# Kernel tuning notes

Measured on AMD Instinct MI355X. Metric: run time of the kernel, lower is better.

Reference implementation:

```python
import jax, jax.numpy as jnp
import numpy as np

DIM, HID, SEQ = 768, 2048, 4096
LR, MOM, WD, THRESH = 1e-3, 0.9, 0.01, 0.1


def _net(p, x):
    W1, b1, W2, b2, W3, b3, W4, b4 = p
    h = jax.nn.relu(x @ W1 + b1)
    h = jax.nn.relu(h @ W2 + b2)
    h = jax.nn.relu(h @ W3 + b3)
    return h @ W4 + b4


def _loss(p, t):
    # t: [dim]; token.unsqueeze(0) then mse_loss (mean over all elements)
    pred = _net(p, t[None, :])
    return jnp.mean((pred - t[None, :]) ** 2)


def _ttt(params, x):
    toks = x[::4]  # `if i % 4 != 0: continue`

    def step(carry, t):
        p, buf, inited = carry
        g = jax.grad(_loss)(p, t)
        surprise = sum(jnp.linalg.norm(gi) for gi in jax.tree_util.tree_leaves(g))
        # momentum buffer: first observation initializes it
        buf_new = jnp.where(inited, MOM * buf + (1.0 - MOM) * surprise, surprise)

        def upd(q):
            qd = jax.tree_util.tree_map(lambda w: w * (1.0 - WD), q)  # weight decay
            g2 = jax.grad(_loss)(qd, t)                                # fresh fwd/bwd
            return jax.tree_util.tree_map(lambda w, gi: w - LR * gi, qd, g2)  # SGD step

        p_new = jax.lax.cond(buf_new > THRESH, upd, lambda q: q, p)
        return (p_new, buf_new, jnp.bool_(True)), None

    (pf, _, _), _ = jax.lax.scan(step, (params, jnp.float32(0.0), jnp.bool_(False)), toks)
    return pf


def setup_inputs() -> dict:
    key = jax.random.key(0)
    ks = jax.random.split(key, 5)

    def lin(k, fi, fo):
        kw, kb = jax.random.split(k)
        w = jax.random.normal(kw, (fi, fo), jnp.float32) / np.sqrt(fi).astype(np.float32)
        b = jax.random.normal(kb, (fo,), jnp.float32) * 0.01
        return w, b

    W1, b1 = lin(ks[0], DIM, HID)
    W2, b2 = lin(ks[1], HID, HID)
    W3, b3 = lin(ks[2], HID, HID)
    W4, b4 = lin(ks[3], HID, DIM)
    x = jax.random.normal(ks[4], (SEQ, DIM), jnp.float32)
    return dict(x=x, W1=W1, b1=b1, W2=W2, b2=b2, W3=W3, b3=b3, W4=W4, b4=b4, do_ttt=1)


def reference(x, W1, b1, W2, b2, W3, b3, W4, b4, do_ttt):
    params = (W1, b1, W2, b2, W3, b3, W4, b4)
    if do_ttt:
        params = _ttt(params, x)
    out = _net(params, x)            # eval pass over full sequence
    return out.mean(axis=0, keepdims=True)  # memory_summary [1, dim]
```

## Files before the change

kernel.cpp:

```cpp
#include <hip/hip_runtime.h>
#include <cstddef>

#define LRC 0.001f
#define DEC 0.99f

typedef float f32x4 __attribute__((ext_vector_type(4)));

static const size_t OFF_H1F = 376832;
static const size_t OFF_H2F = 380928;
static const size_t OFF_H2Q = 382976;
static const size_t OFF_H3F = 385024;
static const size_t OFF_H3Q = 387072;
static const size_t OFF_D4F = 389120;
static const size_t OFF_D4Q = 389888;
static const size_t OFF_D3F = 390656;
static const size_t OFF_D3Q = 392704;
static const size_t OFF_D2F = 394752;
static const size_t OFF_D2Q = 396800;
static const size_t OFF_SL4 = 398848;
static const size_t OFF_D1Q = 400896;
static const size_t OFF_NSQ = 402944;
static const size_t OFF_SL3 = 402960;
static const size_t OFF_SL2 = 403216;
static const size_t OFF_SL1 = 403472;
static const size_t OFF_MSUM = 403732;
static const size_t OFF_HA  = 428308;
static const size_t OFF_HB  = 2525460;

#define ST0  0
#define ST1  2048
#define ST2  4096
#define ST3  6144
#define SD4F 8192
#define SD4Q 8960
#define SRED 9728
#define SCND 10240
#define SBUF 10244
#define SCOND 10245
#define SB4  10248
#define SSQ  10256
#define SWRP 10264
#define SWRQ 10288

__device__ __forceinline__ float clf(const float* p) {
    return __hip_atomic_load(p, __ATOMIC_RELAXED, __HIP_MEMORY_SCOPE_AGENT);
}
__device__ __forceinline__ void csf(float* p, float v) {
    __hip_atomic_store(p, v, __ATOMIC_RELAXED, __HIP_MEMORY_SCOPE_AGENT);
}
__device__ __forceinline__ f32x4 cl4(const float* p) {
    f32x4 r;
    asm volatile("global_load_dwordx4 %0, %1, off sc0 sc1" : "=&v"(r) : "v"(p) : "memory");
    return r;
}
__device__ __forceinline__ void cs4(float* p, f32x4 v) {
    asm volatile("global_store_dwordx4 %0, %1, off sc0 sc1" :: "v"(p), "v"(v) : "memory");
}
__device__ __forceinline__ void vwait() {
    asm volatile("s_waitcnt vmcnt(0)" ::: "memory");
    __builtin_amdgcn_sched_barrier(0);
}

__device__ __forceinline__ float dot4(const f32x4 a, const f32x4 b) {
    float s = a.x * b.x; s += a.y * b.y; s += a.z * b.z; s += a.w * b.w; return s;
}
__device__ __forceinline__ int swz(int p) { return p ^ (((p >> 5) & 7) << 2); }

__device__ __forceinline__ void updc(f32x4& wv, const f32x4 a, float dq) {
    wv.x = DEC * wv.x - (LRC * a.x) * dq;
    wv.y = DEC * wv.y - (LRC * a.y) * dq;
    wv.z = DEC * wv.z - (LRC * a.z) * dq;
    wv.w = DEC * wv.w - (LRC * a.w) * dq;
}
__device__ __forceinline__ void updr(f32x4& wv, float u, const f32x4 dv) {
    wv.x = DEC * wv.x - u * dv.x;
    wv.y = DEC * wv.y - u * dv.y;
    wv.z = DEC * wv.z - u * dv.z;
    wv.w = DEC * wv.w - u * dv.w;
}

__device__ __forceinline__ float block_reduce_512s(float v, float* red) {
    int t = threadIdx.x;
    red[t] = v;
    __syncthreads();
    for (int st = 256; st > 0; st >>= 1) {
        if (t < st) red[t] += red[t + st];
        __syncthreads();
    }
    float r = red[0];
    __syncthreads();
    return r;
}

__device__ __forceinline__ void gbar(unsigned* bar) {
    asm volatile("s_waitcnt vmcnt(0) lgkmcnt(0)" ::: "memory");
    __syncthreads();
    if (threadIdx.x == 0) {
        unsigned g = __hip_atomic_load(bar, __ATOMIC_RELAXED, __HIP_MEMORY_SCOPE_AGENT);
        unsigned* grp = bar + 64 + ((blockIdx.x >> 4) << 5);
        bool released = false;
        if (__hip_atomic_fetch_add(grp, 1u, __ATOMIC_RELAXED, __HIP_MEMORY_SCOPE_AGENT) == 15u) {
            if (__hip_atomic_fetch_add(bar + 32, 1u, __ATOMIC_RELAXED, __HIP_MEMORY_SCOPE_AGENT) == 15u) {
#pragma unroll
                for (int i = 0; i < 16; ++i)
                    __hip_atomic_store(bar + 64 + (i << 5), 0u, __ATOMIC_RELAXED, __HIP_MEMORY_SCOPE_AGENT);
                __hip_atomic_store(bar + 32, 0u, __ATOMIC_RELAXED, __HIP_MEMORY_SCOPE_AGENT);
                __hip_atomic_store(bar, g + 1u, __ATOMIC_RELEASE, __HIP_MEMORY_SCOPE_AGENT);
                released = true;
            }
        }
        if (!released) {
            while (__hip_atomic_load(bar, __ATOMIC_RELAXED, __HIP_MEMORY_SCOPE_AGENT) == g)
                __builtin_amdgcn_s_sleep(2);
            (void)__hip_atomic_load(bar, __ATOMIC_ACQUIRE, __HIP_MEMORY_SCOPE_AGENT);
        }
    }
    __syncthreads();
}

__global__ __launch_bounds__(1024) void k_zero(unsigned* __restrict__ bar) {
    bar[threadIdx.x] = 0u;
}

#define L3M(M) M(0) M(1) M(2)
#define L8M(M) M(0) M(1) M(2) M(3) M(4) M(5) M(6) M(7)
#define LDS_SW(buf, i) (*(const f32x4*)(smem + (buf) + swz(32 * lane + 4 * (i))))
#define LDS_D4(buf, i) (*(const f32x4*)(smem + (buf) + 12 * lane + 4 * (i)))

__global__ void __attribute__((amdgpu_flat_work_group_size(512, 512), amdgpu_waves_per_eu(2, 2)))
k_scan(const float* __restrict__ x,
       float* __restrict__ W1g, float* __restrict__ b1g,
       float* __restrict__ W2g, float* __restrict__ b2g,
       float* __restrict__ W3g, float* __restrict__ b3g,
       float* __restrict__ W4g, float* __restrict__ b4g,
       float* __restrict__ wsf,
       const int* __restrict__ flag) {
    if (*flag == 0) return;
    __shared__ __align__(16) float smem[16896];
    unsigned* bar = (unsigned*)(wsf + OFF_HA);
    const int b = blockIdx.x, tid = threadIdx.x;
    const int w = tid >> 6, lane = tid & 63;
    const int jw = 8 * b + w;
    const int c3 = 3 * b;
    const int t4 = tid * 4;

    f32x4 w1c0, w1c1, w1c2;
    f32x4 w2c0, w2c1, w2c2, w2c3, w2c4, w2c5, w2c6, w2c7;
    f32x4 w3c0, w3c1, w3c2, w3c3, w3c4, w3c5, w3c6, w3c7;
    f32x4 w4c0, w4c1, w4c2;
    f32x4 w4r0, w4r1, w4r2;
    f32x4 w2r0, w2r1, w2r2, w2r3, w2r4, w2r5, w2r6, w2r7;
    f32x4 w3r0, w3r1, w3r2, w3r3, w3r4, w3r5, w3r6, w3r7;

#define LD_COL(dst, Wg, ld, row0, col) { f32x4 t; \
    t.x = Wg[(size_t)((row0) + 0) * (ld) + (col)]; \
    t.y = Wg[(size_t)((row0) + 1) * (ld) + (col)]; \
    t.z = Wg[(size_t)((row0) + 2) * (ld) + (col)]; \
    t.w = Wg[(size_t)((row0) + 3) * (ld) + (col)]; dst = t; }
#define LDW1C(i) LD_COL(w1c##i, W1g, 2048, 12 * lane + 4 * (i), jw)
    L3M(LDW1C)
#undef LDW1C
#define LDW2C(i) LD_COL(w2c##i, W2g, 2048, 32 * lane + 4 * (i), jw)
    L8M(LDW2C)
#undef LDW2C
#define LDW3C(i) LD_COL(w3c##i, W3g, 2048, 32 * lane + 4 * (i), jw)
    L8M(LDW3C)
#undef LDW3C
#define LDW4C(i) LD_COL(w4c##i, W4g, 768, 4 * tid, c3 + (i))
    L3M(LDW4C)
#undef LDW4C
#define LDW4R(i) w4r##i = *(const f32x4*)(W4g + (size_t)jw * 768 + 12 * lane + 4 * (i));
    L3M(LDW4R)
#undef LDW4R
#define LDW2R(i) w2r##i = *(const f32x4*)(W2g + (size_t)jw * 2048 + 32 * lane + 4 * (i));
    L8M(LDW2R)
#undef LDW2R
#define LDW3R(i) w3r##i = *(const f32x4*)(W3g + (size_t)jw * 2048 + 32 * lane + 4 * (i));
    L8M(LDW3R)
#undef LDW3R
    if (tid == 0) smem[SBUF] = 0.f;

    for (int s = 0; s < 1024; ++s) {
        const float* xt = x + (size_t)s * 3072;
        const float* xprev = x + (size_t)(s > 0 ? s - 1 : 0) * 3072;

        float cond = 0.f;
        if (s > 0) {
            if (w < 4) {
                const float* sl = wsf + (w == 0 ? OFF_SL1 : w == 1 ? OFF_SL2 : w == 2 ? OFF_SL3 : OFF_SL4);
                float v = clf(sl + lane) + clf(sl + lane + 64) + clf(sl + lane + 128) + clf(sl + lane + 192);
#pragma unroll
                for (int off = 32; off > 0; off >>= 1) v += __shfl_down(v, off);
                if (lane == 0) smem[SCND + w] = v;
            }
            __syncthreads();
            if (tid == 0) {
                float nd1 = sqrtf(smem[SCND + 0]), nd2 = sqrtf(smem[SCND + 1]);
                float nd3 = sqrtf(smem[SCND + 2]), nd4 = sqrtf(smem[SCND + 3]);
                float nx = sqrtf(clf(wsf + OFF_NSQ + 0));
                float nh1 = sqrtf(clf(wsf + OFF_NSQ + 1));
                float nh2 = sqrtf(clf(wsf + OFF_NSQ + 2));
                float nh3 = sqrtf(clf(wsf + OFF_NSQ + 3));
                float surprise = nx * nd1 + nd1 + nh1 * nd2 + nd2 + nh2 * nd3 + nd3 + nh3 * nd4 + nd4;
                float bufold = smem[SBUF];
                float bufnew = (s == 1) ? surprise : (0.9f * bufold + 0.1f * surprise);
                smem[SBUF] = bufnew;
                smem[SCOND] = (bufnew > 0.1f) ? 1.f : 0.f;
            }
            __syncthreads();
            cond = smem[SCOND];
        }
        float b1j;
        if (cond != 0.f) {
            f32x4 a0 = cl4(wsf + OFF_H1F + t4);
            f32x4 a1 = cl4(wsf + OFF_H2Q + t4);
            f32x4 a2 = cl4(wsf + OFF_D2Q + t4);
            f32x4 a3 = cl4(wsf + OFF_D3Q + t4);
            f32x4 hq3 = cl4(wsf + OFF_H3Q + t4);
            f32x4 d4s = {0.f, 0.f, 0.f, 0.f};
            if (tid < 192) d4s = cl4(wsf + OFF_D4Q + t4);
            float d1qj = clf(wsf + OFF_D1Q + jw);
            float h3qr = clf(wsf + OFF_H3Q + jw);
            float h2qr = clf(wsf + OFF_H2Q + jw);
            float ob1 = b1g[jw];
            f32x4 xp0 = *(const f32x4*)(xprev + 12 * lane);
            f32x4 xp1 = *(const f32x4*)(xprev + 12 * lane + 4);
            f32x4 xp2 = *(const f32x4*)(xprev + 12 * lane + 8);
            vwait();
            {
                int st = swz(t4);
                *(f32x4*)(smem + ST0 + st) = a0;
                *(f32x4*)(smem + ST1 + st) = a1;
                *(f32x4*)(smem + ST2 + st) = a2;
                *(f32x4*)(smem + ST3 + st) = a3;
            }
            if (tid < 192) *(f32x4*)(smem + SD4Q + t4) = d4s;
            __syncthreads();
            updc(w1c0, xp0, d1qj); updc(w1c1, xp1, d1qj); updc(w1c2, xp2, d1qj);
            {
                float d2qj = smem[ST2 + swz(jw)];
#define UPW2C(i) { f32x4 hf = LDS_SW(ST0, i); f32x4 af; \
                   af.x = DEC * hf.x; af.y = DEC * hf.y; af.z = DEC * hf.z; af.w = DEC * hf.w; \
                   updc(w2c##i, af, d2qj); }
                L8M(UPW2C)
#undef UPW2C
            }
            {
                float d3qj = smem[ST3 + swz(jw)];
#define UPW3C(i) { f32x4 hq = LDS_SW(ST1, i); updc(w3c##i, hq, d3qj); }
                L8M(UPW3C)
#undef UPW3C
            }
            {
                float vq0 = smem[SD4Q + c3 + 0];
                float vq1 = smem[SD4Q + c3 + 1];
                float vq2 = smem[SD4Q + c3 + 2];
                updc(w4c0, hq3, vq0); updc(w4c1, hq3, vq1); updc(w4c2, hq3, vq2);
            }
            {
                float u = LRC * h3qr;
#define UPW4R(i) { f32x4 dv = LDS_D4(SD4Q, i); updr(w4r##i, u, dv); }
                L3M(UPW4R)
#undef UPW4R
            }
            {
                float u = LRC * h2qr;
#define UPW3R(i) { f32x4 dv = LDS_SW(ST3, i); updr(w3r##i, u, dv); }
                L8M(UPW3R)
#undef UPW3R
            }
            {
                float u = LRC * (DEC * smem[ST0 + swz(jw)]);
#define UPW2R(i) { f32x4 dv = LDS_SW(ST2, i); updr(w2r##i, u, dv); }
                L8M(UPW2R)
#undef UPW2R
            }
            b1j = DEC * ob1 - LRC * d1qj;
            if (lane == 0) b1g[jw] = b1j;
        } else {
            b1j = b1g[jw];
        }
        {
            f32x4 x0 = *(const f32x4*)(xt + 12 * lane);
            f32x4 x1 = *(const f32x4*)(xt + 12 * lane + 4);
            f32x4 x2 = *(const f32x4*)(xt + 12 * lane + 8);
            float acc = dot4(w1c0, x0);
            acc += dot4(w1c1, x1);
            acc += dot4(w1c2, x2);
#pragma unroll
            for (int off = 32; off > 0; off >>= 1) acc += __shfl_down(acc, off);
            if (lane == 0) csf(wsf + OFF_H1F + jw, fmaxf(acc + b1j, 0.f));
        }
        gbar(bar);

        {
            f32x4 hv = cl4(wsf + OFF_H1F + t4);
            float ob2 = b2g[jw];
            float d2qjo = (cond != 0.f) ? clf(wsf + OFF_D2Q + jw) : 0.f;
            vwait();
            *(f32x4*)(smem + ST0 + swz(t4)) = hv;
            float b2j = (cond != 0.f) ? (DEC * ob2 - LRC * d2qjo) : ob2;
            if (cond != 0.f && lane == 0) b2g[jw] = b2j;
            __syncthreads();
            float accP = 0.f, accQ = 0.f;
#define PHB(i) { const f32x4 hf = LDS_SW(ST0, i); f32x4 hq; \
                 hq.x = DEC * hf.x; hq.y = DEC * hf.y; hq.z = DEC * hf.z; hq.w = DEC * hf.w; \
                 accP += dot4(w2c##i, hf); accQ += dot4(w2c##i, hq); }
            L8M(PHB)
#undef PHB
#pragma unroll
            for (int off = 32; off > 0; off >>= 1) {
                accP += __shfl_down(accP, off);
                accQ += __shfl_down(accQ, off);
            }
            if (lane == 0) {
                csf(wsf + OFF_H2F + jw, fmaxf(accP + b2j, 0.f));
                csf(wsf + OFF_H2Q + jw, fmaxf(DEC * (accQ + b2j), 0.f));
            }
        }
        gbar(bar);

        {
            f32x4 hfv = cl4(wsf + OFF_H2F + t4);
            f32x4 hqv = cl4(wsf + OFF_H2Q + t4);
            float ob3 = b3g[jw];
            float d3qjo = (cond != 0.f) ? clf(wsf + OFF_D3Q + jw) : 0.f;
            vwait();
            {
                int st = swz(t4);
                *(f32x4*)(smem + ST0 + st) = hfv;
                *(f32x4*)(smem + ST1 + st) = hqv;
            }
            float b3j = (cond != 0.f) ? (DEC * ob3 - LRC * d3qjo) : ob3;
            if (cond != 0.f && lane == 0) b3g[jw] = b3j;
            __syncthreads();
            float accP = 0.f, accQ = 0.f;
#define PHC(i) { const f32x4 hf = LDS_SW(ST0, i); const f32x4 hq = LDS_SW(ST1, i); \
                 accP += dot4(w3c##i, hf); accQ += dot4(w3c##i, hq); }
            L8M(PHC)
#undef PHC
#pragma unroll
            for (int off = 32; off > 0; off >>= 1) {
                accP += __shfl_down(accP, off);
                accQ += __shfl_down(accQ, off);
            }
            if (lane == 0) {
                csf(wsf + OFF_H3F + jw, fmaxf(accP + b3j, 0.f));
                csf(wsf + OFF_H3Q + jw, fmaxf(DEC * (accQ + b3j), 0.f));
            }
        }
        gbar(bar);

        {
            f32x4 hfv = cl4(wsf + OFF_H3F + t4);
            f32x4 hqv = cl4(wsf + OFF_H3Q + t4);
            float tv = 0.f;
            if (tid < 3) {
                float ob4 = b4g[c3 + tid];
                float d4qjo = (cond != 0.f) ? clf(wsf + OFF_D4Q + c3 + tid) : 0.f;
                tv = xt[c3 + tid];
                float bn = (cond != 0.f) ? (DEC * ob4 - LRC * d4qjo) : ob4;
                if (cond != 0.f) b4g[c3 + tid] = bn;
                smem[SB4 + tid] = bn;
            }
            vwait();
            {
                int st = swz(t4);
                *(f32x4*)(smem + ST0 + st) = hfv;
                *(f32x4*)(smem + ST1 + st) = hqv;
            }
            float aP0 = dot4(w4c0, hfv), aP1 = dot4(w4c1, hfv), aP2 = dot4(w4c2, hfv);
            float aQ0 = dot4(w4c0, hqv), aQ1 = dot4(w4c1, hqv), aQ2 = dot4(w4c2, hqv);
#pragma unroll
            for (int off = 32; off > 0; off >>= 1) {
                aP0 += __shfl_down(aP0, off); aP1 += __shfl_down(aP1, off); aP2 += __shfl_down(aP2, off);
                aQ0 += __shfl_down(aQ0, off); aQ1 += __shfl_down(aQ1, off); aQ2 += __shfl_down(aQ2, off);
            }
            if (lane == 0) {
                smem[SWRP + w * 3 + 0] = aP0; smem[SWRP + w * 3 + 1] = aP1; smem[SWRP + w * 3 + 2] = aP2;
                smem[SWRQ + w * 3 + 0] = aQ0; smem[SWRQ + w * 3 + 1] = aQ1; smem[SWRQ + w * 3 + 2] = aQ2;
            }
            __syncthreads();
            if (tid < 3) {
                float zp = 0.f, zq = 0.f;
#pragma unroll
                for (int q = 0; q < 8; ++q) { zp += smem[SWRP + q * 3 + tid]; zq += smem[SWRQ + q * 3 + tid]; }
                float bn = smem[SB4 + tid];
                float d4f = 2.f * ((zp + bn) - tv) * (1.f / 768.f);
                float d4q = 2.f * (DEC * (zq + bn) - tv) * (1.f / 768.f);
                csf(wsf + OFF_D4F + c3 + tid, d4f);
                csf(wsf + OFF_D4Q + c3 + tid, d4q);
                smem[SSQ + tid] = d4f * d4f;
            }
            __syncthreads();
            if (tid == 0) csf(wsf + OFF_SL4 + b, smem[SSQ + 0] + smem[SSQ + 1] + smem[SSQ + 2]);
            if (b >= 1 && b <= 4) {
                float v = 0.f;
                if (b == 4) {
                    if (tid < 192) {
                        f32x4 xv = *(const f32x4*)(xt + t4);
                        v = xv.x * xv.x + xv.y * xv.y + xv.z * xv.z + xv.w * xv.w;
                    }
                } else {
                    const float* src = (b == 1) ? wsf + OFF_H1F : (b == 2) ? wsf + OFF_H2F : wsf + OFF_H3F;
                    f32x4 hh = cl4(src + t4);
                    vwait();
                    v = hh.x * hh.x + hh.y * hh.y + hh.z * hh.z + hh.w * hh.w;
                }
                float sres = block_reduce_512s(v, smem + SRED);
                if (tid == 0) csf(wsf + OFF_NSQ + ((b == 4) ? 0 : b), sres);
            }
        }
        gbar(bar);

        {
            f32x4 p4 = {0.f, 0.f, 0.f, 0.f}, q4 = {0.f, 0.f, 0.f, 0.f};
            if (tid < 192) {
                p4 = cl4(wsf + OFF_D4F + t4);
                q4 = cl4(wsf + OFF_D4Q + t4);
            }
            vwait();
            if (tid < 192) {
                *(f32x4*)(smem + SD4F + t4) = p4;
                *(f32x4*)(smem + SD4Q + t4) = q4;
            }
            __syncthreads();
            float accP = 0.f, accQ = 0.f;
#define PHE(i) { const f32x4 dP = LDS_D4(SD4F, i); const f32x4 dQ = LDS_D4(SD4Q, i); \
                 accP += dot4(w4r##i, dP); accQ += dot4(w4r##i, dQ); }
            L3M(PHE)
#undef PHE
#pragma unroll
            for (int off = 32; off > 0; off >>= 1) {
                accP += __shfl_down(accP, off);
                accQ += __shfl_down(accQ, off);
            }
            if (lane == 0) {
                float dp = (smem[ST0 + swz(jw)] > 0.f) ? accP : 0.f;
                float dq = (smem[ST1 + swz(jw)] > 0.f) ? DEC * accQ : 0.f;
                csf(wsf + OFF_D3F + jw, dp);
                csf(wsf + OFF_D3Q + jw, dq);
                smem[SSQ + w] = dp * dp;
            }
            __syncthreads();
            if (tid == 0) {
                float ss = 0.f;
#pragma unroll
                for (int q = 0; q < 8; ++q) ss += smem[SSQ + q];
                csf(wsf + OFF_SL3 + b, ss);
            }
        }
        gbar(bar);

        {
            f32x4 fP = cl4(wsf + OFF_D3F + t4);
            f32x4 fQ = cl4(wsf + OFF_D3Q + t4);
            float h2fr = clf(wsf + OFF_H2F + jw);
            float h2qr = clf(wsf + OFF_H2Q + jw);
            vwait();
            {
                int st = swz(t4);
                *(f32x4*)(smem + ST2 + st) = fP;
                *(f32x4*)(smem + ST3 + st) = fQ;
            }
            __syncthreads();
            float accP = 0.f, accQ = 0.f;
#define PHF(i) { const f32x4 dP = LDS_SW(ST2, i); const f32x4 dQ = LDS_SW(ST3, i); \
                 accP += dot4(w3r##i, dP); accQ += dot4(w3r##i, dQ); }
            L8M(PHF)
#undef PHF
#pragma unroll
            for (int off = 32; off > 0; off >>= 1) {
                accP += __shfl_down(accP, off);
                accQ += __shfl_down(accQ, off);
            }
            if (lane == 0) {
                float dp = (h2fr > 0.f) ? accP : 0.f;
                float dq = (h2qr > 0.f) ? DEC * accQ : 0.f;
                csf(wsf + OFF_D2F + jw, dp);
                csf(wsf + OFF_D2Q + jw, dq);
                smem[SSQ + w] = dp * dp;
            }
            __syncthreads();
            if (tid == 0) {
                float ss = 0.f;
#pragma unroll
                for (int q = 0; q < 8; ++q) ss += smem[SSQ + q];
                csf(wsf + OFF_SL2 + b, ss);
            }
        }
        gbar(bar);

        {
            f32x4 fP = cl4(wsf + OFF_D2F + t4);
            f32x4 fQ = cl4(wsf + OFF_D2Q + t4);
            float h1fr = clf(wsf + OFF_H1F + jw);
            vwait();
            {
                int st = swz(t4);
                *(f32x4*)(smem + ST0 + st) = fP;
                *(f32x4*)(smem + ST1 + st) = fQ;
            }
            __syncthreads();
            float accP = 0.f, accQ = 0.f;
#define PHG(i) { const f32x4 dP = LDS_SW(ST0, i); const f32x4 dQ = LDS_SW(ST1, i); \
                 accP += dot4(w2r##i, dP); accQ += dot4(w2r##i, dQ); }
            L8M(PHG)
#undef PHG
#pragma unroll
            for (int off = 32; off > 0; off >>= 1) {
                accP += __shfl_down(accP, off);
                accQ += __shfl_down(accQ, off);
            }
            if (lane == 0) {
                float dp = (h1fr > 0.f) ? accP : 0.f;
                float h1qr = DEC * h1fr;
                float dq = (h1qr > 0.f) ? DEC * accQ : 0.f;
                csf(wsf + OFF_D1Q + jw, dq);
                smem[SSQ + w] = dp * dp;
            }
            __syncthreads();
            if (tid == 0) {
                float ss = 0.f;
#pragma unroll
                for (int q = 0; q < 8; ++q) ss += smem[SSQ + q];
                csf(wsf + OFF_SL1 + b, ss);
            }
        }
        gbar(bar);
    }

    {
        if (w < 4) {
            const float* sl = wsf + (w == 0 ? OFF_SL1 : w == 1 ? OFF_SL2 : w == 2 ? OFF_SL3 : OFF_SL4);
            float v = clf(sl + lane) + clf(sl + lane + 64) + clf(sl + lane + 128) + clf(sl + lane + 192);
#pragma unroll
            for (int off = 32; off > 0; off >>= 1) v += __shfl_down(v, off);
            if (lane == 0) smem[SCND + w] = v;
        }
        __syncthreads();
        if (tid == 0) {
            float nd1 = sqrtf(smem[SCND + 0]), nd2 = sqrtf(smem[SCND + 1]);
            float nd3 = sqrtf(smem[SCND + 2]), nd4 = sqrtf(smem[SCND + 3]);
            float nx = sqrtf(clf(wsf + OFF_NSQ + 0));
            float nh1 = sqrtf(clf(wsf + OFF_NSQ + 1));
            float nh2 = sqrtf(clf(wsf + OFF_NSQ + 2));
            float nh3 = sqrtf(clf(wsf + OFF_NSQ + 3));
            float surprise = nx * nd1 + nd1 + nh1 * nd2 + nd2 + nh2 * nd3 + nd3 + nh3 * nd4 + nd4;
            float bufnew = 0.9f * smem[SBUF] + 0.1f * surprise;
            smem[SCOND] = (bufnew > 0.1f) ? 1.f : 0.f;
        }
        __syncthreads();
        if (smem[SCOND] != 0.f) {
            const float* xpE = x + (size_t)1023 * 3072;
            f32x4 a0 = cl4(wsf + OFF_H1F + t4);
            f32x4 a1 = cl4(wsf + OFF_H2Q + t4);
            f32x4 hq3 = cl4(wsf + OFF_H3Q + t4);
            f32x4 d4s = {0.f, 0.f, 0.f, 0.f};
            if (tid < 192) d4s = cl4(wsf + OFF_D4Q + t4);
            float d1qj = clf(wsf + OFF_D1Q + jw);
            float d2qj = clf(wsf + OFF_D2Q + jw);
            float d3qj = clf(wsf + OFF_D3Q + jw);
            f32x4 xp0 = *(const f32x4*)(xpE + 12 * lane);
            f32x4 xp1 = *(const f32x4*)(xpE + 12 * lane + 4);
            f32x4 xp2 = *(const f32x4*)(xpE + 12 * lane + 8);
            vwait();
            {
                int st = swz(t4);
                *(f32x4*)(smem + ST0 + st) = a0;
                *(f32x4*)(smem + ST1 + st) = a1;
            }
            if (tid < 192) *(f32x4*)(smem + SD4Q + t4) = d4s;
            __syncthreads();
            updc(w1c0, xp0, d1qj); updc(w1c1, xp1, d1qj); updc(w1c2, xp2, d1qj);
#define EPW2C(i) { f32x4 hf = LDS_SW(ST0, i); f32x4 af; \
                   af.x = DEC * hf.x; af.y = DEC * hf.y; af.z = DEC * hf.z; af.w = DEC * hf.w; \
                   updc(w2c##i, af, d2qj); }
            L8M(EPW2C)
#undef EPW2C
#define EPW3C(i) { f32x4 hq = LDS_SW(ST1, i); updc(w3c##i, hq, d3qj); }
            L8M(EPW3C)
#undef EPW3C
            {
                float vq0 = smem[SD4Q + c3 + 0];
                float vq1 = smem[SD4Q + c3 + 1];
                float vq2 = smem[SD4Q + c3 + 2];
                updc(w4c0, hq3, vq0); updc(w4c1, hq3, vq1); updc(w4c2, hq3, vq2);
            }
            if (lane == 0) {
                b1g[jw] = DEC * b1g[jw] - LRC * d1qj;
                b2g[jw] = DEC * b2g[jw] - LRC * d2qj;
                b3g[jw] = DEC * b3g[jw] - LRC * d3qj;
            }
            if (tid < 3) b4g[c3 + tid] = DEC * b4g[c3 + tid] - LRC * smem[SD4Q + c3 + tid];
        }
    }

    __syncthreads();
    {
#define WBW2(i) { smem[(32 * lane + 4 * (i) + 0) * 8 + w] = w2c##i.x; \
                  smem[(32 * lane + 4 * (i) + 1) * 8 + w] = w2c##i.y; \
                  smem[(32 * lane + 4 * (i) + 2) * 8 + w] = w2c##i.z; \
                  smem[(32 * lane + 4 * (i) + 3) * 8 + w] = w2c##i.w; }
        L8M(WBW2)
#undef WBW2
        __syncthreads();
#pragma unroll
        for (int r2 = 0; r2 < 4; ++r2) {
            int r = t4 + r2;
            *(f32x4*)(W2g + (size_t)r * 2048 + 8 * b) = *(const f32x4*)(smem + r * 8);
            *(f32x4*)(W2g + (size_t)r * 2048 + 8 * b + 4) = *(const f32x4*)(smem + r * 8 + 4);
        }
        __syncthreads();
    }
    {
#define WBW3(i) { smem[(32 * lane + 4 * (i) + 0) * 8 + w] = w3c##i.x; \
                  smem[(32 * lane + 4 * (i) + 1) * 8 + w] = w3c##i.y; \
                  smem[(32 * lane + 4 * (i) + 2) * 8 + w] = w3c##i.z; \
                  smem[(32 * lane + 4 * (i) + 3) * 8 + w] = w3c##i.w; }
        L8M(WBW3)
#undef WBW3
        __syncthreads();
#pragma unroll
        for (int r2 = 0; r2 < 4; ++r2) {
            int r = t4 + r2;
            *(f32x4*)(W3g + (size_t)r * 2048 + 8 * b) = *(const f32x4*)(smem + r * 8);
            *(f32x4*)(W3g + (size_t)r * 2048 + 8 * b + 4) = *(const f32x4*)(smem + r * 8 + 4);
        }
        __syncthreads();
    }
    {
#define WBW1(i) { smem[(12 * lane + 4 * (i) + 0) * 8 + w] = w1c##i.x; \
                  smem[(12 * lane + 4 * (i) + 1) * 8 + w] = w1c##i.y; \
                  smem[(12 * lane + 4 * (i) + 2) * 8 + w] = w1c##i.z; \
                  smem[(12 * lane + 4 * (i) + 3) * 8 + w] = w1c##i.w; }
        L3M(WBW1)
#undef WBW1
        __syncthreads();
        for (int r = tid; r < 768; r += 512) {
            *(f32x4*)(W1g + (size_t)r * 2048 + 8 * b) = *(const f32x4*)(smem + r * 8);
            *(f32x4*)(W1g + (size_t)r * 2048 + 8 * b + 4) = *(const f32x4*)(smem + r * 8 + 4);
        }
        __syncthreads();
    }
    {
#define WBW4(c) { smem[(4 * tid + 0) * 3 + (c)] = w4c##c.x; \
                  smem[(4 * tid + 1) * 3 + (c)] = w4c##c.y; \
                  smem[(4 * tid + 2) * 3 + (c)] = w4c##c.z; \
                  smem[(4 * tid + 3) * 3 + (c)] = w4c##c.w; }
        L3M(WBW4)
#undef WBW4
        __syncthreads();
#pragma unroll
        for (int r2 = 0; r2 < 4; ++r2) {
            int r = t4 + r2;
            W4g[(size_t)r * 768 + c3 + 0] = smem[r * 3 + 0];
            W4g[(size_t)r * 768 + c3 + 1] = smem[r * 3 + 1];
            W4g[(size_t)r * 768 + c3 + 2] = smem[r * 3 + 2];
        }
    }
}

__global__ __launch_bounds__(256) void k_gemm(const float* __restrict__ A,
                                              const float* __restrict__ W,
                                              const float* __restrict__ bias,
                                              float* __restrict__ C,
                                              int M, int N, int K, int do_relu) {
    __shared__ float sA[16][64];
    __shared__ float sB[16][128];
    int bn = blockIdx.x, bm = blockIdx.y;
    int m0 = bm * 64, n0 = bn * 128;
    int tid = threadIdx.x;
    int tx = tid & 31, ty = tid >> 5;
    float acc[8][4];
#pragma unroll
    for (int i = 0; i < 8; ++i)
#pragma unroll
        for (int j = 0; j < 4; ++j) acc[i][j] = 0.f;

    for (int kt = 0; kt < K; kt += 16) {
        {
            int r = tid >> 2, cc = (tid & 3) * 4;
            const float4 a4 = *(const float4*)(A + (size_t)(m0 + r) * K + kt + cc);
            sA[cc + 0][r] = a4.x; sA[cc + 1][r] = a4.y; sA[cc + 2][r] = a4.z; sA[cc + 3][r] = a4.w;
        }
        {
            int r = tid >> 5, cc = (tid & 31) * 4;
            *(float4*)(&sB[r][cc]) = *(const float4*)(W + (size_t)(kt + r) * N + n0 + cc);
            *(float4*)(&sB[r + 8][cc]) = *(const float4*)(W + (size_t)(kt + r + 8) * N + n0 + cc);
        }
        __syncthreads();
#pragma unroll
        for (int k = 0; k < 16; ++k) {
            float av[8];
#pragma unroll
            for (int i = 0; i < 8; ++i) av[i] = sA[k][ty * 8 + i];
            float bx = sB[k][tx * 4 + 0], by = sB[k][tx * 4 + 1];
            float bz = sB[k][tx * 4 + 2], bw = sB[k][tx * 4 + 3];
#pragma unroll
            for (int i = 0; i < 8; ++i) {
                acc[i][0] += av[i] * bx; acc[i][1] += av[i] * by;
                acc[i][2] += av[i] * bz; acc[i][3] += av[i] * bw;
            }
        }
        __syncthreads();
    }
    float bx = bias[n0 + tx * 4 + 0], by = bias[n0 + tx * 4 + 1];
    float bz = bias[n0 + tx * 4 + 2], bw = bias[n0 + tx * 4 + 3];
#pragma unroll
    for (int i = 0; i < 8; ++i) {
        int m = m0 + ty * 8 + i;
        float4 v;
        v.x = acc[i][0] + bx; v.y = acc[i][1] + by;
        v.z = acc[i][2] + bz; v.w = acc[i][3] + bw;
        if (do_relu) {
            v.x = fmaxf(v.x, 0.f); v.y = fmaxf(v.y, 0.f);
            v.z = fmaxf(v.z, 0.f); v.w = fmaxf(v.w, 0.f);
        }
        *(float4*)(C + (size_t)m * N + n0 + tx * 4) = v;
    }
}

__global__ __launch_bounds__(128) void k_colsum(const float* __restrict__ Y,
                                                float* __restrict__ out) {
    int c = blockIdx.x * 128 + threadIdx.x;
    int r0 = blockIdx.y * 128;
    float s = 0.f;
    for (int r = 0; r < 128; ++r) s += Y[(size_t)(r0 + r) * 768 + c];
    out[blockIdx.y * 768 + c] = s;
}

__global__ __launch_bounds__(768) void k_out(const float* __restrict__ msum,
                                             float* __restrict__ out) {
    int c = threadIdx.x;
    float s = 0.f;
#pragma unroll
    for (int i = 0; i < 32; ++i) s += msum[i * 768 + c];
    out[c] = s * (1.f / 4096.f);
}

extern "C" void kernel_launch(void* const* d_in, const int* in_sizes, int n_in,
                              void* d_out, int out_size, void* d_ws, size_t ws_size,
                              hipStream_t stream) {
    const float* x = (const float*)d_in[0];
    float* W1 = (float*)d_in[1];
    float* b1 = (float*)d_in[2];
    float* W2 = (float*)d_in[3];
    float* b2 = (float*)d_in[4];
    float* W3 = (float*)d_in[5];
    float* b3 = (float*)d_in[6];
    float* W4 = (float*)d_in[7];
    float* b4 = (float*)d_in[8];
    const int* flag = (const int*)d_in[9];
    float* wsf = (float*)d_ws;

    unsigned* bar = (unsigned*)(wsf + OFF_HA);
    k_zero<<<1, 1024, 0, stream>>>(bar);

    k_scan<<<256, 512, 0, stream>>>(x, W1, b1, W2, b2, W3, b3, W4, b4, wsf, flag);

    float* HA = wsf + OFF_HA;
    float* HB = wsf + OFF_HB;
    for (int ch = 0; ch < 4; ++ch) {
        const float* Xc = x + (size_t)ch * 1024 * 768;
        k_gemm<<<dim3(16, 16), 256, 0, stream>>>(Xc, W1, b1, HA, 1024, 2048, 768, 1);
        k_gemm<<<dim3(16, 16), 256, 0, stream>>>(HA, W2, b2, HB, 1024, 2048, 2048, 1);
        k_gemm<<<dim3(16, 16), 256, 0, stream>>>(HB, W3, b3, HA, 1024, 2048, 2048, 1);
        k_gemm<<<dim3(6, 16), 256, 0, stream>>>(HA, W4, b4, HB, 1024, 768, 2048, 0);
        k_colsum<<<dim3(6, 8), 128, 0, stream>>>(HB, wsf + OFF_MSUM + (size_t)ch * 8 * 768);
    }
    k_out<<<1, 768, 0, stream>>>(wsf + OFF_MSUM, (float*)d_out);
}
```

Measured before the change: 66.14 ms.

## Keep per-step activations and deltas resident in LDS instead of reloading from global

The shared-memory layout is reorganized so that activation vectors (h1, h2, h3) and backprop deltas (d2, d3, d4, d1 per-wave) stay in dedicated LDS slots across phases of the persistent scan kernel. The weight-update phase and several bias and norm computations now read these from LDS rather than issuing coherent global loads plus a vwait and a staging barrier. This is meant to cut global round-trips and one block-wide sync per step on the serial critical path. It raises LDS usage per block and adds an extra vmcnt wait inside the grid barrier.

```diff
diff --git a/kernel.cpp b/kernel.cpp
--- a/kernel.cpp
+++ b/kernel.cpp
@@ -27,20 +27,25 @@
 static const size_t OFF_HA  = 428308;
 static const size_t OFF_HB  = 2525460;
 
-#define ST0  0
-#define ST1  2048
-#define ST2  4096
-#define ST3  6144
-#define SD4F 8192
-#define SD4Q 8960
-#define SRED 9728
-#define SCND 10240
-#define SBUF 10244
-#define SCOND 10245
-#define SB4  10248
-#define SSQ  10256
-#define SWRP 10264
-#define SWRQ 10288
+#define PH1F 0
+#define PH2F 2048
+#define PH2Q 4096
+#define PH3Q 6144
+#define PD2Q 8192
+#define PD3Q 10240
+#define PD4Q 12288
+#define SD4F 13056
+#define ST0  13824
+#define ST2  15872
+#define SRED 17920
+#define SCND 18432
+#define SBUF 18436
+#define SCOND 18437
+#define SB4  18440
+#define SSQ  18448
+#define SWRP 18456
+#define SWRQ 18480
+#define PD1W 18504
 
 __device__ __forceinline__ float clf(const float* p) {
     return __hip_atomic_load(p, __ATOMIC_RELAXED, __HIP_MEMORY_SCOPE_AGENT);
@@ -52,9 +57,6 @@
     f32x4 r;
     asm volatile("global_load_dwordx4 %0, %1, off sc0 sc1" : "=&v"(r) : "v"(p) : "memory");
     return r;
-}
-__device__ __forceinline__ void cs4(float* p, f32x4 v) {
-    asm volatile("global_store_dwordx4 %0, %1, off sc0 sc1" :: "v"(p), "v"(v) : "memory");
 }
 __device__ __forceinline__ void vwait() {
     asm volatile("s_waitcnt vmcnt(0)" ::: "memory");
@@ -97,6 +99,7 @@
     __syncthreads();
     if (threadIdx.x == 0) {
         unsigned g = __hip_atomic_load(bar, __ATOMIC_RELAXED, __HIP_MEMORY_SCOPE_AGENT);
+        asm volatile("s_waitcnt vmcnt(0)" ::: "memory");
         unsigned* grp = bar + 64 + ((blockIdx.x >> 4) << 5);
         bool released = false;
         if (__hip_atomic_fetch_add(grp, 1u, __ATOMIC_RELAXED, __HIP_MEMORY_SCOPE_AGENT) == 15u) {
@@ -127,16 +130,16 @@
 #define LDS_SW(buf, i) (*(const f32x4*)(smem + (buf) + swz(32 * lane + 4 * (i))))
 #define LDS_D4(buf, i) (*(const f32x4*)(smem + (buf) + 12 * lane + 4 * (i)))
 
-__global__ void __attribute__((amdgpu_flat_work_group_size(512, 512), amdgpu_waves_per_eu(2, 2)))
-k_scan(const float* __restrict__ x,
-       float* __restrict__ W1g, float* __restrict__ b1g,
-       float* __restrict__ W2g, float* __restrict__ b2g,
-       float* __restrict__ W3g, float* __restrict__ b3g,
-       float* __restrict__ W4g, float* __restrict__ b4g,
-       float* __restrict__ wsf,
-       const int* __restrict__ flag) {
+__global__ __attribute__((amdgpu_flat_work_group_size(512, 512), amdgpu_waves_per_eu(2, 2)))
+void k_scan(const float* __restrict__ x,
+            float* __restrict__ W1g, float* __restrict__ b1g,
+            float* __restrict__ W2g, float* __restrict__ b2g,
+            float* __restrict__ W3g, float* __restrict__ b3g,
+            float* __restrict__ W4g, float* __restrict__ b4g,
+            float* __restrict__ wsf,
+            const int* __restrict__ flag) {
     if (*flag == 0) return;
-    __shared__ __align__(16) float smem[16896];
+    __shared__ __align__(16) float smem[18512];
     unsigned* bar = (unsigned*)(wsf + OFF_HA);
     const int b = blockIdx.x, tid = threadIdx.x;
     const int w = tid >> 6, lane = tid & 63;
@@ -212,66 +215,48 @@
         }
         float b1j;
         if (cond != 0.f) {
-            f32x4 a0 = cl4(wsf + OFF_H1F + t4);
-            f32x4 a1 = cl4(wsf + OFF_H2Q + t4);
-            f32x4 a2 = cl4(wsf + OFF_D2Q + t4);
-            f32x4 a3 = cl4(wsf + OFF_D3Q + t4);
-            f32x4 hq3 = cl4(wsf + OFF_H3Q + t4);
-            f32x4 d4s = {0.f, 0.f, 0.f, 0.f};
-            if (tid < 192) d4s = cl4(wsf + OFF_D4Q + t4);
-            float d1qj = clf(wsf + OFF_D1Q + jw);
-            float h3qr = clf(wsf + OFF_H3Q + jw);
-            float h2qr = clf(wsf + OFF_H2Q + jw);
             float ob1 = b1g[jw];
             f32x4 xp0 = *(const f32x4*)(xprev + 12 * lane);
             f32x4 xp1 = *(const f32x4*)(xprev + 12 * lane + 4);
             f32x4 xp2 = *(const f32x4*)(xprev + 12 * lane + 8);
-            vwait();
-            {
-                int st = swz(t4);
-                *(f32x4*)(smem + ST0 + st) = a0;
-                *(f32x4*)(smem + ST1 + st) = a1;
-                *(f32x4*)(smem + ST2 + st) = a2;
-                *(f32x4*)(smem + ST3 + st) = a3;
-            }
-            if (tid < 192) *(f32x4*)(smem + SD4Q + t4) = d4s;
-            __syncthreads();
+            float d1qj = smem[PD1W + w];
             updc(w1c0, xp0, d1qj); updc(w1c1, xp1, d1qj); updc(w1c2, xp2, d1qj);
             {
-                float d2qj = smem[ST2 + swz(jw)];
-#define UPW2C(i) { f32x4 hf = LDS_SW(ST0, i); f32x4 af; \
+                float d2qj = smem[PD2Q + swz(jw)];
+#define UPW2C(i) { f32x4 hf = LDS_SW(PH1F, i); f32x4 af; \
                    af.x = DEC * hf.x; af.y = DEC * hf.y; af.z = DEC * hf.z; af.w = DEC * hf.w; \
                    updc(w2c##i, af, d2qj); }
                 L8M(UPW2C)
 #undef UPW2C
             }
             {
-                float d3qj = smem[ST3 + swz(jw)];
-#define UPW3C(i) { f32x4 hq = LDS_SW(ST1, i); updc(w3c##i, hq, d3qj); }
+                float d3qj = smem[PD3Q + swz(jw)];
+#define UPW3C(i) { f32x4 hq = LDS_SW(PH2Q, i); updc(w3c##i, hq, d3qj); }
                 L8M(UPW3C)
 #undef UPW3C
             }
             {
-                float vq0 = smem[SD4Q + c3 + 0];
-                float vq1 = smem[SD4Q + c3 + 1];
-                float vq2 = smem[SD4Q + c3 + 2];
+                f32x4 hq3 = *(const f32x4*)(smem + PH3Q + swz(t4));
+                float vq0 = smem[PD4Q + c3 + 0];
+                float vq1 = smem[PD4Q + c3 + 1];
+                float vq2 = smem[PD4Q + c3 + 2];
                 updc(w4c0, hq3, vq0); updc(w4c1, hq3, vq1); updc(w4c2, hq3, vq2);
             }
             {
-                float u = LRC * h3qr;
-#define UPW4R(i) { f32x4 dv = LDS_D4(SD4Q, i); updr(w4r##i, u, dv); }
+                float u = LRC * smem[PH3Q + swz(jw)];
+#define UPW4R(i) { f32x4 dv = LDS_D4(PD4Q, i); updr(w4r##i, u, dv); }
                 L3M(UPW4R)
 #undef UPW4R
             }
             {
-                float u = LRC * h2qr;
-#define UPW3R(i) { f32x4 dv = LDS_SW(ST3, i); updr(w3r##i, u, dv); }
+                float u = LRC * smem[PH2Q + swz(jw)];
+#define UPW3R(i) { f32x4 dv = LDS_SW(PD3Q, i); updr(w3r##i, u, dv); }
                 L8M(UPW3R)
 #undef UPW3R
             }
             {
-                float u = LRC * (DEC * smem[ST0 + swz(jw)]);
-#define UPW2R(i) { f32x4 dv = LDS_SW(ST2, i); updr(w2r##i, u, dv); }
+                float u = LRC * (DEC * smem[PH1F + swz(jw)]);
+#define UPW2R(i) { f32x4 dv = LDS_SW(PD2Q, i); updr(w2r##i, u, dv); }
                 L8M(UPW2R)
 #undef UPW2R
             }
@@ -296,14 +281,14 @@
         {
             f32x4 hv = cl4(wsf + OFF_H1F + t4);
             float ob2 = b2g[jw];
-            float d2qjo = (cond != 0.f) ? clf(wsf + OFF_D2Q + jw) : 0.f;
+            float d2qjo = (cond != 0.f) ? smem[PD2Q + swz(jw)] : 0.f;
             vwait();
-            *(f32x4*)(smem + ST0 + swz(t4)) = hv;
+            *(f32x4*)(smem + PH1F + swz(t4)) = hv;
             float b2j = (cond != 0.f) ? (DEC * ob2 - LRC * d2qjo) : ob2;
             if (cond != 0.f && lane == 0) b2g[jw] = b2j;
             __syncthreads();
             float accP = 0.f, accQ = 0.f;
-#define PHB(i) { const f32x4 hf = LDS_SW(ST0, i); f32x4 hq; \
+#define PHB(i) { const f32x4 hf = LDS_SW(PH1F, i); f32x4 hq; \
                  hq.x = DEC * hf.x; hq.y = DEC * hf.y; hq.z = DEC * hf.z; hq.w = DEC * hf.w; \
                  accP += dot4(w2c##i, hf); accQ += dot4(w2c##i, hq); }
             L8M(PHB)
@@ -324,18 +309,18 @@
             f32x4 hfv = cl4(wsf + OFF_H2F + t4);
             f32x4 hqv = cl4(wsf + OFF_H2Q + t4);
             float ob3 = b3g[jw];
-            float d3qjo = (cond != 0.f) ? clf(wsf + OFF_D3Q + jw) : 0.f;
+            float d3qjo = (cond != 0.f) ? smem[PD3Q + swz(jw)] : 0.f;
             vwait();
             {
                 int st = swz(t4);
-                *(f32x4*)(smem + ST0 + st) = hfv;
-                *(f32x4*)(smem + ST1 + st) = hqv;
+                *(f32x4*)(smem + PH2F + st) = hfv;
+                *(f32x4*)(smem + PH2Q + st) = hqv;
             }
             float b3j = (cond != 0.f) ? (DEC * ob3 - LRC * d3qjo) : ob3;
             if (cond != 0.f && lane == 0) b3g[jw] = b3j;
             __syncthreads();
             float accP = 0.f, accQ = 0.f;
-#define PHC(i) { const f32x4 hf = LDS_SW(ST0, i); const f32x4 hq = LDS_SW(ST1, i); \
+#define PHC(i) { const f32x4 hf = LDS_SW(PH2F, i); const f32x4 hq = LDS_SW(PH2Q, i); \
                  accP += dot4(w3c##i, hf); accQ += dot4(w3c##i, hq); }
             L8M(PHC)
 #undef PHC
@@ -357,7 +342,7 @@
             float tv = 0.f;
             if (tid < 3) {
                 float ob4 = b4g[c3 + tid];
-                float d4qjo = (cond != 0.f) ? clf(wsf + OFF_D4Q + c3 + tid) : 0.f;
+                float d4qjo = (cond != 0.f) ? smem[PD4Q + c3 + tid] : 0.f;
                 tv = xt[c3 + tid];
                 float bn = (cond != 0.f) ? (DEC * ob4 - LRC * d4qjo) : ob4;
                 if (cond != 0.f) b4g[c3 + tid] = bn;
@@ -367,7 +352,7 @@
             {
                 int st = swz(t4);
                 *(f32x4*)(smem + ST0 + st) = hfv;
-                *(f32x4*)(smem + ST1 + st) = hqv;
+                *(f32x4*)(smem + PH3Q + st) = hqv;
             }
             float aP0 = dot4(w4c0, hfv), aP1 = dot4(w4c1, hfv), aP2 = dot4(w4c2, hfv);
             float aQ0 = dot4(w4c0, hqv), aQ1 = dot4(w4c1, hqv), aQ2 = dot4(w4c2, hqv);
@@ -402,9 +387,8 @@
                         v = xv.x * xv.x + xv.y * xv.y + xv.z * xv.z + xv.w * xv.w;
                     }
                 } else {
-                    const float* src = (b == 1) ? wsf + OFF_H1F : (b == 2) ? wsf + OFF_H2F : wsf + OFF_H3F;
-                    f32x4 hh = cl4(src + t4);
-                    vwait();
+                    const int so = (b == 1) ? PH1F : (b == 2) ? PH2F : ST0;
+                    f32x4 hh = *(const f32x4*)(smem + so + swz(t4));
                     v = hh.x * hh.x + hh.y * hh.y + hh.z * hh.z + hh.w * hh.w;
                 }
                 float sres = block_reduce_512s(v, smem + SRED);
@@ -422,11 +406,11 @@
             vwait();
             if (tid < 192) {
                 *(f32x4*)(smem + SD4F + t4) = p4;
-                *(f32x4*)(smem + SD4Q + t4) = q4;
+                *(f32x4*)(smem + PD4Q + t4) = q4;
             }
             __syncthreads();
             float accP = 0.f, accQ = 0.f;
-#define PHE(i) { const f32x4 dP = LDS_D4(SD4F, i); const f32x4 dQ = LDS_D4(SD4Q, i); \
+#define PHE(i) { const f32x4 dP = LDS_D4(SD4F, i); const f32x4 dQ = LDS_D4(PD4Q, i); \
                  accP += dot4(w4r##i, dP); accQ += dot4(w4r##i, dQ); }
             L3M(PHE)
 #undef PHE
@@ -437,7 +421,7 @@
             }
             if (lane == 0) {
                 float dp = (smem[ST0 + swz(jw)] > 0.f) ? accP : 0.f;
-                float dq = (smem[ST1 + swz(jw)] > 0.f) ? DEC * accQ : 0.f;
+                float dq = (smem[PH3Q + swz(jw)] > 0.f) ? DEC * accQ : 0.f;
                 csf(wsf + OFF_D3F + jw, dp);
                 csf(wsf + OFF_D3Q + jw, dq);
                 smem[SSQ + w] = dp * dp;
@@ -455,17 +439,17 @@
         {
             f32x4 fP = cl4(wsf + OFF_D3F + t4);
             f32x4 fQ = cl4(wsf + OFF_D3Q + t4);
-            float h2fr = clf(wsf + OFF_H2F + jw);
-            float h2qr = clf(wsf + OFF_H2Q + jw);
+            float h2fr = smem[PH2F + swz(jw)];
+            float h2qr = smem[PH2Q + swz(jw)];
             vwait();
             {
                 int st = swz(t4);
                 *(f32x4*)(smem + ST2 + st) = fP;
-                *(f32x4*)(smem + ST3 + st) = fQ;
+                *(f32x4*)(smem + PD3Q + st) = fQ;
             }
             __syncthreads();
             float accP = 0.f, accQ = 0.f;
-#define PHF(i) { const f32x4 dP = LDS_SW(ST2, i); const f32x4 dQ = LDS_SW(ST3, i); \
+#define PHF(i) { const f32x4 dP = LDS_SW(ST2, i); const f32x4 dQ = LDS_SW(PD3Q, i); \
                  accP += dot4(w3r##i, dP); accQ += dot4(w3r##i, dQ); }
             L8M(PHF)
 #undef PHF
@@ -494,16 +478,16 @@
         {
             f32x4 fP = cl4(wsf + OFF_D2F + t4);
             f32x4 fQ = cl4(wsf + OFF_D2Q + t4);
-            float h1fr = clf(wsf + OFF_H1F + jw);
+            float h1fr = smem[PH1F + swz(jw)];
             vwait();
             {
                 int st = swz(t4);
                 *(f32x4*)(smem + ST0 + st) = fP;
-                *(f32x4*)(smem + ST1 + st) = fQ;
+                *(f32x4*)(smem + PD2Q + st) = fQ;
             }
             __syncthreads();
             float accP = 0.f, accQ = 0.f;
-#define PHG(i) { const f32x4 dP = LDS_SW(ST0, i); const f32x4 dQ = LDS_SW(ST1, i); \
+#define PHG(i) { const f32x4 dP = LDS_SW(ST0, i); const f32x4 dQ = LDS_SW(PD2Q, i); \
                  accP += dot4(w2r##i, dP); accQ += dot4(w2r##i, dQ); }
             L8M(PHG)
 #undef PHG
@@ -517,6 +501,7 @@
                 float h1qr = DEC * h1fr;
                 float dq = (h1qr > 0.f) ? DEC * accQ : 0.f;
                 csf(wsf + OFF_D1Q + jw, dq);
+                smem[PD1W + w] = dq;
                 smem[SSQ + w] = dp * dp;
             }
             __syncthreads();
@@ -553,38 +538,26 @@
         __syncthreads();
         if (smem[SCOND] != 0.f) {
             const float* xpE = x + (size_t)1023 * 3072;
-            f32x4 a0 = cl4(wsf + OFF_H1F + t4);
-            f32x4 a1 = cl4(wsf + OFF_H2Q + t4);
-            f32x4 hq3 = cl4(wsf + OFF_H3Q + t4);
-            f32x4 d4s = {0.f, 0.f, 0.f, 0.f};
-            if (tid < 192) d4s = cl4(wsf + OFF_D4Q + t4);
-            float d1qj = clf(wsf + OFF_D1Q + jw);
-            float d2qj = clf(wsf + OFF_D2Q + jw);
-            float d3qj = clf(wsf + OFF_D3Q + jw);
             f32x4 xp0 = *(const f32x4*)(xpE + 12 * lane);
             f32x4 xp1 = *(const f32x4*)(xpE + 12 * lane + 4);
             f32x4 xp2 = *(const f32x4*)(xpE + 12 * lane + 8);
-            vwait();
-            {
-                int st = swz(t4);
-                *(f32x4*)(smem + ST0 + st) = a0;
-                *(f32x4*)(smem + ST1 + st) = a1;
-            }
-            if (tid < 192) *(f32x4*)(smem + SD4Q + t4) = d4s;
-            __syncthreads();
+            float d1qj = smem[PD1W + w];
             updc(w1c0, xp0, d1qj); updc(w1c1, xp1, d1qj); updc(w1c2, xp2, d1qj);
-#define EPW2C(i) { f32x4 hf = LDS_SW(ST0, i); f32x4 af; \
+            float d2qj = smem[PD2Q + swz(jw)];
+            float d3qj = smem[PD3Q + swz(jw)];
+#define EPW2C(i) { f32x4 hf = LDS_SW(PH1F, i); f32x4 af; \
                    af.x = DEC * hf.x; af.y = DEC * hf.y; af.z = DEC * hf.z; af.w = DEC * hf.w; \
                    updc(w2c##i, af, d2qj); }
             L8M(EPW2C)
 #undef EPW2C
-#define EPW3C(i) { f32x4 hq = LDS_SW(ST1, i); updc(w3c##i, hq, d3qj); }
+#define EPW3C(i) { f32x4 hq = LDS_SW(PH2Q, i); updc(w3c##i, hq, d3qj); }
             L8M(EPW3C)
 #undef EPW3C
             {
-                float vq0 = smem[SD4Q + c3 + 0];
-                float vq1 = smem[SD4Q + c3 + 1];
-                float vq2 = smem[SD4Q + c3 + 2];
+                f32x4 hq3 = *(const f32x4*)(smem + PH3Q + swz(t4));
+                float vq0 = smem[PD4Q + c3 + 0];
+                float vq1 = smem[PD4Q + c3 + 1];
+                float vq2 = smem[PD4Q + c3 + 2];
                 updc(w4c0, hq3, vq0); updc(w4c1, hq3, vq1); updc(w4c2, hq3, vq2);
             }
             if (lane == 0) {
@@ -592,7 +565,7 @@
                 b2g[jw] = DEC * b2g[jw] - LRC * d2qj;
                 b3g[jw] = DEC * b3g[jw] - LRC * d3qj;
             }
-            if (tid < 3) b4g[c3 + tid] = DEC * b4g[c3 + tid] - LRC * smem[SD4Q + c3 + tid];
+            if (tid < 3) b4g[c3 + tid] = DEC * b4g[c3 + tid] - LRC * smem[PD4Q + c3 + tid];
         }
     }
 
```

Result: faster. 60.26 ms (-8.9%).
